# Kernel optimization log

Measured on AMD Instinct MI355X. Metric: run time of the kernel, lower is better.

## Reference

```python
import jax, jax.numpy as jnp
import numpy as np

N_NODES = 100000
N_EDGES = 1600000
BN_EPS = 1e-5
NUM_LAYER = 20


def setup_inputs() -> dict:
    key = jax.random.key(0)
    ks = jax.random.split(key, 10)
    inp = {
        "M": jax.random.normal(ks[0], (N_NODES, 3), dtype=jnp.float32),
        "H": jax.random.normal(ks[1], (N_EDGES, 3), dtype=jnp.float32),
        "edge_index": jax.random.randint(ks[2], (2, N_EDGES), 0, N_NODES, dtype=jnp.int32),
        # mlp_e: Linear(9,4) -> BN(4) -> ReLU -> Linear(4,3)
        "we_w1": jax.random.normal(ks[3], (9, 4), dtype=jnp.float32) * 0.3,
        "we_b1": jnp.zeros((4,), jnp.float32),
        "we_g1": jnp.ones((4,), jnp.float32),
        "we_be1": jnp.zeros((4,), jnp.float32),
        "we_w2": jax.random.normal(ks[4], (4, 3), dtype=jnp.float32) * 0.3,
        "we_b2": jnp.zeros((3,), jnp.float32),
        # mlp_v: Linear(6,3) -> BN(3) -> ReLU -> Linear(3,3)
        "wv_w1": jax.random.normal(ks[5], (6, 3), dtype=jnp.float32) * 0.3,
        "wv_b1": jnp.zeros((3,), jnp.float32),
        "wv_g1": jnp.ones((3,), jnp.float32),
        "wv_be1": jnp.zeros((3,), jnp.float32),
        "wv_w2": jax.random.normal(ks[6], (3, 3), dtype=jnp.float32) * 0.3,
        "wv_b2": jnp.zeros((3,), jnp.float32),
        # head: Linear(3,3) -> BN(3) -> ReLU -> Linear(3,2) -> Softmax
        "out_w1": jax.random.normal(ks[7], (3, 3), dtype=jnp.float32) * 0.3,
        "out_b1": jnp.zeros((3,), jnp.float32),
        "out_g": jnp.ones((3,), jnp.float32),
        "out_be": jnp.zeros((3,), jnp.float32),
        "out_w2": jax.random.normal(ks[8], (3, 2), dtype=jnp.float32) * 0.3,
        "out_b2": jnp.zeros((2,), jnp.float32),
    }
    return inp


def _bn(x, g, b):
    # BatchNorm1d in training mode: batch stats, biased variance
    m = jnp.mean(x, axis=0)
    v = jnp.mean(jnp.square(x - m), axis=0)
    return (x - m) * jax.lax.rsqrt(v + BN_EPS) * g + b


def reference(M, H, edge_index, we_w1, we_b1, we_g1, we_be1, we_w2, we_b2,
              wv_w1, wv_b1, wv_g1, wv_be1, wv_w2, wv_b2,
              out_w1, out_b1, out_g, out_be, out_w2, out_b2):
    src = edge_index[0]  # _j (source, flow=source_to_target)
    dst = edge_index[1]  # _i (target), also the aggregation index
    n = M.shape[0]

    def layer(carry, _):
        M, H = carry
        Mi = M[dst]  # [E,3] gather of target node feats
        Mj = M[src]  # [E,3] gather of source node feats
        e_in = jnp.concatenate([Mi, Mj, H], axis=1)  # [E,9]
        Hn = jax.nn.relu(_bn(e_in @ we_w1 + we_b1, we_g1, we_be1)) @ we_w2 + we_b2  # [E,3]
        v_in = jnp.concatenate([Mi, Hn], axis=1)  # [E,6]
        Mmsg = jax.nn.relu(_bn(v_in @ wv_w1 + wv_b1, wv_g1, wv_be1)) @ wv_w2 + wv_b2  # [E,3]
        Mn = jax.ops.segment_sum(Mmsg, dst, num_segments=n)  # scatter-add to targets
        return (Mn, Hn), None

    (M, H), _ = jax.lax.scan(layer, (M, H), None, length=NUM_LAYER)
    logits = jax.nn.relu(_bn(H @ out_w1 + out_b1, out_g, out_be)) @ out_w2 + out_b2  # [E,2]
    return jax.nn.softmax(logits, axis=1)
```

## Files before the change

kernel.cpp:

```cpp
#include <hip/hip_runtime.h>
#include <hip/hip_fp16.h>
#include <math.h>

#define NNODES 100000
#define NEDGES 1600000
#define NGROUP (NEDGES / 4)
#define NLAYERS 20
#define NB 256
#define BLK 256
#define GRIDE 1024
#define STRIDE (GRIDE * BLK)
#define GRIDL ((NGROUP + BLK - 1) / BLK)
#define NBLKN ((NNODES + 255) / 256)
#define GRIDN4 ((NNODES * 4 + BLK - 1) / BLK)

struct __align__(8) H4 { __half h[4]; };

template<int N>
__device__ __forceinline__ void block_stats_atomic(const float* vals, double* base) {
  __shared__ double sm[16][4];
  int lane = threadIdx.x & 63, wid = threadIdx.x >> 6;
  __syncthreads();
  #pragma unroll
  for (int n = 0; n < N; ++n) {
    double d = (double)vals[n];
    #pragma unroll
    for (int o = 32; o > 0; o >>= 1) d += __shfl_down(d, o, 64);
    if (lane == 0) sm[n][wid] = d;
  }
  __syncthreads();
  if (threadIdx.x < N) {
    double s = sm[threadIdx.x][0] + sm[threadIdx.x][1] + sm[threadIdx.x][2] + sm[threadIdx.x][3];
    atomicAdd(base + threadIdx.x, s);
  }
}

template<int NS>
__device__ __forceinline__ void bank_reduce(const double* __restrict__ acc, double* res) {
  __shared__ double red[BLK * 8];
  int t = threadIdx.x;
  #pragma unroll
  for (int s = 0; s < NS; ++s) red[t * 8 + s] = acc[t * 8 + s];
  __syncthreads();
  for (int o = BLK / 2; o > 0; o >>= 1) {
    if (t < o) {
      #pragma unroll
      for (int s = 0; s < NS; ++s) red[t * 8 + s] += red[(t + o) * 8 + s];
    }
    __syncthreads();
  }
  #pragma unroll
  for (int s = 0; s < NS; ++s) res[s] = red[s];
  __syncthreads();
}

__device__ __forceinline__ void compute_x(const float4 mi, const float4 mj,
    float h0, float h1, float h2,
    const float* __restrict__ w, const float* __restrict__ b, float* x) {
  #pragma unroll
  for (int j = 0; j < 4; ++j) {
    float t = b[j];
    t += mi.x * w[0 * 4 + j]; t += mi.y * w[1 * 4 + j]; t += mi.z * w[2 * 4 + j];
    t += mj.x * w[3 * 4 + j]; t += mj.y * w[4 * 4 + j]; t += mj.z * w[5 * 4 + j];
    t += h0 * w[6 * 4 + j];  t += h1 * w[7 * 4 + j];  t += h2 * w[8 * 4 + j];
    x[j] = t;
  }
}

__global__ void __launch_bounds__(BLK) kz(const float* __restrict__ Min,
                                          float* __restrict__ M,
                                          int* __restrict__ hist,
                                          double* __restrict__ accs) {
  int tid = blockIdx.x * BLK + threadIdx.x;
  for (int v = tid; v < NNODES; v += STRIDE) {
    float4 m;
    m.x = Min[3 * v]; m.y = Min[3 * v + 1]; m.z = Min[3 * v + 2]; m.w = 0.f;
    *(float4*)(M + 4 * (size_t)v) = m;
    hist[v] = 0;
  }
  for (int i = tid; i < 3 * NB * 8; i += STRIDE) accs[i] = 0.0;
}

__global__ void __launch_bounds__(BLK) khr(const int* __restrict__ dst,
                                           int* __restrict__ hist,
                                           int* __restrict__ rankpos) {
  int g = blockIdx.x * BLK + threadIdx.x;
  if (g >= NGROUP) return;
  int4 d4 = ((const int4*)dst)[g];
  int4 r;
  r.x = atomicAdd(&hist[d4.x], 1);
  r.y = atomicAdd(&hist[d4.y], 1);
  r.z = atomicAdd(&hist[d4.z], 1);
  r.w = atomicAdd(&hist[d4.w], 1);
  ((int4*)rankpos)[g] = r;
}

__global__ void __launch_bounds__(256) ksA(const int* __restrict__ hist,
                                           int* __restrict__ bsum) {
  __shared__ int sm[256];
  int i = blockIdx.x * 256 + threadIdx.x;
  sm[threadIdx.x] = (i < NNODES) ? hist[i] : 0;
  __syncthreads();
  for (int o = 128; o > 0; o >>= 1) {
    if (threadIdx.x < o) sm[threadIdx.x] += sm[threadIdx.x + o];
    __syncthreads();
  }
  if (threadIdx.x == 0) bsum[blockIdx.x] = sm[0];
}

__global__ void __launch_bounds__(512) ksB(const int* __restrict__ bsum,
                                           int* __restrict__ bbase) {
  __shared__ int sm[512];
  int t = threadIdx.x;
  sm[t] = (t < NBLKN) ? bsum[t] : 0;
  __syncthreads();
  for (int o = 1; o < 512; o <<= 1) {
    int v = (t >= o) ? sm[t - o] : 0;
    __syncthreads();
    sm[t] += v;
    __syncthreads();
  }
  if (t < NBLKN) bbase[t] = (t == 0) ? 0 : sm[t - 1];
}

__global__ void __launch_bounds__(256) ksC(const int* __restrict__ hist,
                                           const int* __restrict__ bbase,
                                           int* __restrict__ off) {
  __shared__ int sm[256];
  int t = threadIdx.x;
  int i = blockIdx.x * 256 + t;
  int v = (i < NNODES) ? hist[i] : 0;
  sm[t] = v;
  __syncthreads();
  for (int o = 1; o < 256; o <<= 1) {
    int u = (t >= o) ? sm[t - o] : 0;
    __syncthreads();
    sm[t] += u;
    __syncthreads();
  }
  if (i < NNODES) off[i] = bbase[blockIdx.x] + sm[t] - v;
  if (i == 0) off[NNODES] = NEDGES;
}

__global__ void __launch_bounds__(BLK) kd(const int* __restrict__ off,
                                          int* __restrict__ dp) {
  int v = blockIdx.x * BLK + threadIdx.x;
  if (v >= NNODES) return;
  int e0 = off[v], e1 = off[v + 1];
  for (int e = e0; e < e1; ++e) dp[e] = v;
}

__global__ void __launch_bounds__(BLK) kp1(const int* __restrict__ dst,
                                           const int* __restrict__ off,
                                           int* __restrict__ rankpos,
                                           int* __restrict__ eperm) {
  int g = blockIdx.x * BLK + threadIdx.x;
  if (g >= NGROUP) return;
  int4 d4 = ((const int4*)dst)[g];
  int4 r4 = ((int4*)rankpos)[g];
  int4 p4;
  p4.x = off[d4.x] + r4.x;
  p4.y = off[d4.y] + r4.y;
  p4.z = off[d4.z] + r4.z;
  p4.w = off[d4.w] + r4.w;
  int e = 4 * g;
  eperm[p4.x] = e; eperm[p4.y] = e + 1; eperm[p4.z] = e + 2; eperm[p4.w] = e + 3;
  ((int4*)rankpos)[g] = p4;
}

__global__ void __launch_bounds__(BLK) kp2(const int* __restrict__ src,
                                           const float* __restrict__ Hin,
                                           const int* __restrict__ eperm,
                                           int* __restrict__ sp,
                                           __half* __restrict__ Hp) {
  int g = blockIdx.x * BLK + threadIdx.x;
  if (g >= NGROUP) return;
  int4 e4 = ((const int4*)eperm)[g];
  int4 s4;
  s4.x = src[e4.x];
  s4.y = src[e4.y];
  s4.z = src[e4.z];
  s4.w = src[e4.w];
  __half hh[12];
  int ee[4] = {e4.x, e4.y, e4.z, e4.w};
  #pragma unroll
  for (int k = 0; k < 4; ++k) {
    size_t e3 = 3 * (size_t)ee[k];
    hh[3 * k]     = __float2half(Hin[e3]);
    hh[3 * k + 1] = __float2half(Hin[e3 + 1]);
    hh[3 * k + 2] = __float2half(Hin[e3 + 2]);
  }
  ((int4*)sp)[g] = s4;
  H4* Hv = (H4*)(Hp + 12 * (size_t)g);
  H4 a, b, c;
  #pragma unroll
  for (int i = 0; i < 4; ++i) { a.h[i] = hh[i]; b.h[i] = hh[4 + i]; c.h[i] = hh[8 + i]; }
  Hv[0] = a; Hv[1] = b; Hv[2] = c;
}

__global__ void __launch_bounds__(BLK) k1(
    const float* __restrict__ M, const __half* __restrict__ H,
    const int* __restrict__ sp, const int* __restrict__ dp,
    const float* __restrict__ W1, const float* __restrict__ b1,
    double* __restrict__ acc1, double* __restrict__ acc2) {
  int g = blockIdx.x * BLK + threadIdx.x;
  if (blockIdx.x == 0)
    for (int i = threadIdx.x; i < NB * 8; i += BLK) acc2[i] = 0.0;

  float sx[4] = {0, 0, 0, 0}, sq[4] = {0, 0, 0, 0};
  if (g < NGROUP) {
    int4 s4 = ((const int4*)sp)[g];
    int4 d4 = ((const int4*)dp)[g];
    const H4* Hv = (const H4*)(H + 12 * (size_t)g);
    H4 a = Hv[0], b = Hv[1], c = Hv[2];
    float hf[12];
    #pragma unroll
    for (int i = 0; i < 4; ++i) {
      hf[i] = __half2float(a.h[i]); hf[4 + i] = __half2float(b.h[i]); hf[8 + i] = __half2float(c.h[i]);
    }
    float4 mi0 = *(const float4*)(M + 4 * (size_t)d4.x);
    float4 mj0 = *(const float4*)(M + 4 * (size_t)s4.x);
    float4 mi1 = *(const float4*)(M + 4 * (size_t)d4.y);
    float4 mj1 = *(const float4*)(M + 4 * (size_t)s4.y);
    float4 mi2 = *(const float4*)(M + 4 * (size_t)d4.z);
    float4 mj2 = *(const float4*)(M + 4 * (size_t)s4.z);
    float4 mi3 = *(const float4*)(M + 4 * (size_t)d4.w);
    float4 mj3 = *(const float4*)(M + 4 * (size_t)s4.w);
    float x[4][4];
    compute_x(mi0, mj0, hf[0], hf[1], hf[2],  W1, b1, x[0]);
    compute_x(mi1, mj1, hf[3], hf[4], hf[5],  W1, b1, x[1]);
    compute_x(mi2, mj2, hf[6], hf[7], hf[8],  W1, b1, x[2]);
    compute_x(mi3, mj3, hf[9], hf[10], hf[11], W1, b1, x[3]);
    #pragma unroll
    for (int k = 0; k < 4; ++k)
      #pragma unroll
      for (int j = 0; j < 4; ++j) { sx[j] += x[k][j]; sq[j] += x[k][j] * x[k][j]; }
  }
  float vals[8] = {sx[0], sx[1], sx[2], sx[3], sq[0], sq[1], sq[2], sq[3]};
  block_stats_atomic<8>(vals, acc1 + (size_t)(blockIdx.x & (NB - 1)) * 8);
}

__global__ void __launch_bounds__(BLK) k2(
    const float* __restrict__ M, const __half* __restrict__ H, __half* __restrict__ Hn,
    const int* __restrict__ sp, const int* __restrict__ dp,
    const float* __restrict__ W1, const float* __restrict__ b1,
    const float* __restrict__ g1, const float* __restrict__ be1,
    const float* __restrict__ W2, const float* __restrict__ b2,
    const float* __restrict__ V1, const float* __restrict__ vb1,
    const double* __restrict__ acc1, double* __restrict__ acc2,
    int isFinal,
    const float* __restrict__ OW1, const float* __restrict__ ob1,
    double* __restrict__ accF) {
  double red[8];
  bank_reduce<8>(acc1, red);
  float s1[4], t1[4];
  {
    const double invE = 1.0 / (double)NEDGES;
    #pragma unroll
    for (int j = 0; j < 4; ++j) {
      double m = red[j] * invE;
      double var = red[4 + j] * invE - m * m;
      double sc = (double)g1[j] / sqrt(var + 1e-5);
      s1[j] = (float)sc;
      t1[j] = (float)((double)be1[j] - m * sc);
    }
  }
  float sz[3] = {0, 0, 0}, szz[3] = {0, 0, 0}, sf[3] = {0, 0, 0}, sff[3] = {0, 0, 0};
  int g = blockIdx.x * BLK + threadIdx.x;
  if (g < NGROUP) {
    int4 s4 = ((const int4*)sp)[g];
    int4 d4 = ((const int4*)dp)[g];
    const H4* Hv = (const H4*)(H + 12 * (size_t)g);
    H4 ha = Hv[0], hb = Hv[1], hc = Hv[2];
    float hf[12];
    #pragma unroll
    for (int i = 0; i < 4; ++i) {
      hf[i] = __half2float(ha.h[i]); hf[4 + i] = __half2float(hb.h[i]); hf[8 + i] = __half2float(hc.h[i]);
    }
    float4 mi[4], mj[4];
    mi[0] = *(const float4*)(M + 4 * (size_t)d4.x);
    mj[0] = *(const float4*)(M + 4 * (size_t)s4.x);
    mi[1] = *(const float4*)(M + 4 * (size_t)d4.y);
    mj[1] = *(const float4*)(M + 4 * (size_t)s4.y);
    mi[2] = *(const float4*)(M + 4 * (size_t)d4.z);
    mj[2] = *(const float4*)(M + 4 * (size_t)s4.z);
    mi[3] = *(const float4*)(M + 4 * (size_t)d4.w);
    mj[3] = *(const float4*)(M + 4 * (size_t)s4.w);
    __half hh[12];
    float hnr[4][3];
    #pragma unroll
    for (int k = 0; k < 4; ++k) {
      float x[4], y[4];
      compute_x(mi[k], mj[k], hf[3 * k], hf[3 * k + 1], hf[3 * k + 2], W1, b1, x);
      #pragma unroll
      for (int j = 0; j < 4; ++j) y[j] = fmaxf(x[j] * s1[j] + t1[j], 0.f);
      #pragma unroll
      for (int c = 0; c < 3; ++c) {
        float v = b2[c] + y[0] * W2[0 * 3 + c] + y[1] * W2[1 * 3 + c]
                        + y[2] * W2[2 * 3 + c] + y[3] * W2[3 * 3 + c];
        __half hv = __float2half(v);
        hh[3 * k + c] = hv;
        hnr[k][c] = __half2float(hv);
      }
      #pragma unroll
      for (int c = 0; c < 3; ++c) {
        float z = vb1[c] + mi[k].x * V1[0 * 3 + c] + mi[k].y * V1[1 * 3 + c] + mi[k].z * V1[2 * 3 + c]
                         + hnr[k][0] * V1[3 * 3 + c] + hnr[k][1] * V1[4 * 3 + c] + hnr[k][2] * V1[5 * 3 + c];
        sz[c] += z; szz[c] += z * z;
      }
      if (isFinal) {
        #pragma unroll
        for (int c = 0; c < 3; ++c) {
          float f = ob1[c] + hnr[k][0] * OW1[0 * 3 + c] + hnr[k][1] * OW1[1 * 3 + c] + hnr[k][2] * OW1[2 * 3 + c];
          sf[c] += f; sff[c] += f * f;
        }
      }
    }
    H4* Hw = (H4*)(Hn + 12 * (size_t)g);
    H4 oA, oB, oC;
    #pragma unroll
    for (int i = 0; i < 4; ++i) { oA.h[i] = hh[i]; oB.h[i] = hh[4 + i]; oC.h[i] = hh[8 + i]; }
    Hw[0] = oA; Hw[1] = oB; Hw[2] = oC;
  }
  size_t bank = (size_t)(blockIdx.x & (NB - 1)) * 8;
  float v6[6] = {sz[0], sz[1], sz[2], szz[0], szz[1], szz[2]};
  block_stats_atomic<6>(v6, acc2 + bank);
  if (isFinal) {
    float v6b[6] = {sf[0], sf[1], sf[2], sff[0], sff[1], sff[2]};
    block_stats_atomic<6>(v6b, accF + bank);
  }
}

__global__ void __launch_bounds__(BLK) k3(
    const float* __restrict__ M, const __half* __restrict__ Hn,
    const int* __restrict__ off,
    const float* __restrict__ V1, const float* __restrict__ vb1,
    const float* __restrict__ vg1, const float* __restrict__ vbe1,
    const float* __restrict__ V2, const float* __restrict__ vb2,
    const double* __restrict__ acc2, double* __restrict__ acc1,
    float* __restrict__ Mnew) {
  double red[6];
  bank_reduce<6>(acc2, red);
  float s2[3], t2[3];
  {
    const double invE = 1.0 / (double)NEDGES;
    #pragma unroll
    for (int c = 0; c < 3; ++c) {
      double m = red[c] * invE;
      double var = red[3 + c] * invE - m * m;
      double sc = (double)vg1[c] / sqrt(var + 1e-5);
      s2[c] = (float)sc;
      t2[c] = (float)((double)vbe1[c] - m * sc);
    }
  }
  if (blockIdx.x == 0)
    for (int i = threadIdx.x; i < NB * 8; i += BLK) acc1[i] = 0.0;

  int idx = blockIdx.x * BLK + threadIdx.x;
  int v = idx >> 2, q = idx & 3;
  if (v >= NNODES) return;
  float4 mi = *(const float4*)(M + 4 * (size_t)v);
  int e0 = off[v], e1 = off[v + 1];
  float a0 = 0.f, a1 = 0.f, a2v = 0.f;
  for (int e = e0 + q; e < e1; e += 4) {
    size_t e3 = 3 * (size_t)e;
    float h0 = __half2float(Hn[e3]), h1 = __half2float(Hn[e3 + 1]), h2 = __half2float(Hn[e3 + 2]);
    float y[3];
    #pragma unroll
    for (int c = 0; c < 3; ++c) {
      float z = vb1[c] + mi.x * V1[0 * 3 + c] + mi.y * V1[1 * 3 + c] + mi.z * V1[2 * 3 + c]
                       + h0 * V1[3 * 3 + c] + h1 * V1[4 * 3 + c] + h2 * V1[5 * 3 + c];
      y[c] = fmaxf(z * s2[c] + t2[c], 0.f);
    }
    a0  += vb2[0] + y[0] * V2[0] + y[1] * V2[3] + y[2] * V2[6];
    a1  += vb2[1] + y[0] * V2[1] + y[1] * V2[4] + y[2] * V2[7];
    a2v += vb2[2] + y[0] * V2[2] + y[1] * V2[5] + y[2] * V2[8];
  }
  a0  += __shfl_down(a0, 2, 4);  a0  += __shfl_down(a0, 1, 4);
  a1  += __shfl_down(a1, 2, 4);  a1  += __shfl_down(a1, 1, 4);
  a2v += __shfl_down(a2v, 2, 4); a2v += __shfl_down(a2v, 1, 4);
  if (q == 0) {
    float4 o; o.x = a0; o.y = a1; o.z = a2v; o.w = 0.f;
    *(float4*)(Mnew + 4 * (size_t)v) = o;
  }
}

__global__ void __launch_bounds__(BLK) f2(
    const __half* __restrict__ H, const int* __restrict__ pos,
    const float* __restrict__ OW1, const float* __restrict__ ob1,
    const float* __restrict__ og, const float* __restrict__ obe,
    const float* __restrict__ OW2, const float* __restrict__ ob2,
    const double* __restrict__ accF, float* __restrict__ out) {
  double red[6];
  bank_reduce<6>(accF, red);
  float sF[3], tF[3];
  {
    const double invE = 1.0 / (double)NEDGES;
    #pragma unroll
    for (int c = 0; c < 3; ++c) {
      double m = red[c] * invE;
      double var = red[3 + c] * invE - m * m;
      double sc = (double)og[c] / sqrt(var + 1e-5);
      sF[c] = (float)sc;
      tF[c] = (float)((double)obe[c] - m * sc);
    }
  }
  int g = blockIdx.x * BLK + threadIdx.x;
  if (g >= NGROUP) return;
  int4 p4 = ((const int4*)pos)[g];
  int p[4] = {p4.x, p4.y, p4.z, p4.w};
  float2 o[4];
  #pragma unroll
  for (int k = 0; k < 4; ++k) {
    size_t p3 = 3 * (size_t)p[k];
    float h0 = __half2float(H[p3]), h1 = __half2float(H[p3 + 1]), h2 = __half2float(H[p3 + 2]);
    float y[3];
    #pragma unroll
    for (int c = 0; c < 3; ++c) {
      float f = ob1[c] + h0 * OW1[0 * 3 + c] + h1 * OW1[1 * 3 + c] + h2 * OW1[2 * 3 + c];
      y[c] = fmaxf(f * sF[c] + tF[c], 0.f);
    }
    float l0 = ob2[0] + y[0] * OW2[0] + y[1] * OW2[2] + y[2] * OW2[4];
    float l1 = ob2[1] + y[0] * OW2[1] + y[1] * OW2[3] + y[2] * OW2[5];
    float mx = fmaxf(l0, l1);
    float e0 = __expf(l0 - mx), e1 = __expf(l1 - mx);
    float inv = 1.f / (e0 + e1);
    o[k].x = e0 * inv; o[k].y = e1 * inv;
  }
  float4 oA, oB;
  oA.x = o[0].x; oA.y = o[0].y; oA.z = o[1].x; oA.w = o[1].y;
  oB.x = o[2].x; oB.y = o[2].y; oB.z = o[3].x; oB.w = o[3].y;
  ((float4*)out)[2 * (size_t)g] = oA;
  ((float4*)out)[2 * (size_t)g + 1] = oB;
}

extern "C" void kernel_launch(void* const* d_in, const int* in_sizes, int n_in,
                              void* d_out, int out_size, void* d_ws, size_t ws_size,
                              hipStream_t stream) {
  const float* M_in   = (const float*)d_in[0];
  const float* H_in   = (const float*)d_in[1];
  const int*   ei     = (const int*)d_in[2];
  const float* we_w1  = (const float*)d_in[3];
  const float* we_b1  = (const float*)d_in[4];
  const float* we_g1  = (const float*)d_in[5];
  const float* we_be1 = (const float*)d_in[6];
  const float* we_w2  = (const float*)d_in[7];
  const float* we_b2  = (const float*)d_in[8];
  const float* wv_w1  = (const float*)d_in[9];
  const float* wv_b1  = (const float*)d_in[10];
  const float* wv_g1  = (const float*)d_in[11];
  const float* wv_be1 = (const float*)d_in[12];
  const float* wv_w2  = (const float*)d_in[13];
  const float* wv_b2  = (const float*)d_in[14];
  const float* out_w1 = (const float*)d_in[15];
  const float* out_b1 = (const float*)d_in[16];
  const float* out_g  = (const float*)d_in[17];
  const float* out_be = (const float*)d_in[18];
  const float* out_w2 = (const float*)d_in[19];
  const float* out_b2 = (const float*)d_in[20];
  const int* src = ei;
  const int* dst = ei + NEDGES;

  float* ws = (float*)d_ws;
  float* MA  = ws;
  float* MB  = ws + 400000;
  __half* Hp0 = (__half*)(ws + 800000);
  __half* Hp1 = (__half*)(ws + 3200000);
  int* eperm  = (int*)Hp1;
  int* ib      = (int*)(ws + 5600000);
  int* sp      = ib;
  int* dp      = ib + 1600000;
  int* rankpos = ib + 3200000;
  int* hist    = ib + 4800000;
  int* off     = ib + 4900000;
  int* bsum    = ib + 5000001;
  int* bbase   = ib + 5000401;
  double* accs = (double*)(ws + 5600000 + 5000802);
  double* acc1 = accs;
  double* acc2 = accs + NB * 8;
  double* accF = accs + 2 * NB * 8;

  kz<<<GRIDE, BLK, 0, stream>>>(M_in, MA, hist, accs);
  khr<<<GRIDL, BLK, 0, stream>>>(dst, hist, rankpos);
  ksA<<<NBLKN, 256, 0, stream>>>(hist, bsum);
  ksB<<<1, 512, 0, stream>>>(bsum, bbase);
  ksC<<<NBLKN, 256, 0, stream>>>(hist, bbase, off);
  kd<<<NBLKN, BLK, 0, stream>>>(off, dp);
  kp1<<<GRIDL, BLK, 0, stream>>>(dst, off, rankpos, eperm);
  kp2<<<GRIDL, BLK, 0, stream>>>(src, H_in, eperm, sp, Hp0);

  for (int l = 0; l < NLAYERS; ++l) {
    const float* Mc = (l & 1) ? MB : MA;
    float*       Mn = (l & 1) ? MA : MB;
    const __half* Hc = (l & 1) ? Hp1 : Hp0;
    __half*       Hw = (l & 1) ? Hp0 : Hp1;
    k1<<<GRIDL, BLK, 0, stream>>>(Mc, Hc, sp, dp, we_w1, we_b1, acc1, acc2);
    k2<<<GRIDL, BLK, 0, stream>>>(Mc, Hc, Hw, sp, dp, we_w1, we_b1, we_g1, we_be1,
                                  we_w2, we_b2, wv_w1, wv_b1, acc1, acc2,
                                  (l == NLAYERS - 1) ? 1 : 0, out_w1, out_b1, accF);
    if (l < NLAYERS - 1)
      k3<<<GRIDN4, BLK, 0, stream>>>(
          Mc, Hw, off, wv_w1, wv_b1, wv_g1, wv_be1, wv_w2, wv_b2, acc2, acc1, Mn);
  }
  f2<<<GRIDL, BLK, 0, stream>>>(Hp0, rankpos, out_w1, out_b1, out_g, out_be,
                                out_w2, out_b2, accF, (float*)d_out);
}
```

Before: 1.224 ms.

## Delta-pack sorted destination indices and use wave-shuffle bank reduction

Destination indices, which are sorted by CSR order, are packed per group of four as a base plus three 8-bit deltas (int2 instead of int4), halving the dst index traffic read by k1 and k2 on every layer. The dp fill is merged into the scan kernel ksC, removing the separate kd launch, and a new kpk kernel builds the packed array once. bank_reduce replaces the shared-memory tree reduction with wave shuffles plus a 4-entry partial sum, cutting barriers and shared memory. The packing assumes in-group deltas fit in 8 bits, which holds because dp is sorted and a node would need over 255 in-degree gaps to break it; in fact deltas are bounded by node gaps within four consecutive sorted edges, which could exceed 255 only with long runs of empty nodes.

```diff
diff --git a/kernel.cpp b/kernel.cpp
--- a/kernel.cpp
+++ b/kernel.cpp
@@ -37,21 +37,23 @@
 
 template<int NS>
 __device__ __forceinline__ void bank_reduce(const double* __restrict__ acc, double* res) {
-  __shared__ double red[BLK * 8];
+  __shared__ double part[4][8];
   int t = threadIdx.x;
-  #pragma unroll
-  for (int s = 0; s < NS; ++s) red[t * 8 + s] = acc[t * 8 + s];
+  double v[NS];
+  #pragma unroll
+  for (int s = 0; s < NS; ++s) v[s] = acc[t * 8 + s];
+  #pragma unroll
+  for (int o = 32; o > 0; o >>= 1)
+    #pragma unroll
+    for (int s = 0; s < NS; ++s) v[s] += __shfl_down(v[s], o, 64);
+  if ((t & 63) == 0) {
+    int w = t >> 6;
+    #pragma unroll
+    for (int s = 0; s < NS; ++s) part[w][s] = v[s];
+  }
   __syncthreads();
-  for (int o = BLK / 2; o > 0; o >>= 1) {
-    if (t < o) {
-      #pragma unroll
-      for (int s = 0; s < NS; ++s) red[t * 8 + s] += red[(t + o) * 8 + s];
-    }
-    __syncthreads();
-  }
-  #pragma unroll
-  for (int s = 0; s < NS; ++s) res[s] = red[s];
-  __syncthreads();
+  #pragma unroll
+  for (int s = 0; s < NS; ++s) res[s] = part[0][s] + part[1][s] + part[2][s] + part[3][s];
 }
 
 __device__ __forceinline__ void compute_x(const float4 mi, const float4 mj,
@@ -125,7 +127,8 @@
 
 __global__ void __launch_bounds__(256) ksC(const int* __restrict__ hist,
                                            const int* __restrict__ bbase,
-                                           int* __restrict__ off) {
+                                           int* __restrict__ off,
+                                           int* __restrict__ dp) {
   __shared__ int sm[256];
   int t = threadIdx.x;
   int i = blockIdx.x * 256 + t;
@@ -138,16 +141,23 @@
     sm[t] += u;
     __syncthreads();
   }
-  if (i < NNODES) off[i] = bbase[blockIdx.x] + sm[t] - v;
+  if (i < NNODES) {
+    int ex = bbase[blockIdx.x] + sm[t] - v;
+    off[i] = ex;
+    for (int e = ex; e < ex + v; ++e) dp[e] = i;
+  }
   if (i == 0) off[NNODES] = NEDGES;
 }
 
-__global__ void __launch_bounds__(BLK) kd(const int* __restrict__ off,
-                                          int* __restrict__ dp) {
-  int v = blockIdx.x * BLK + threadIdx.x;
-  if (v >= NNODES) return;
-  int e0 = off[v], e1 = off[v + 1];
-  for (int e = e0; e < e1; ++e) dp[e] = v;
+__global__ void __launch_bounds__(BLK) kpk(const int* __restrict__ dp,
+                                           int2* __restrict__ dpp) {
+  int g = blockIdx.x * BLK + threadIdx.x;
+  if (g >= NGROUP) return;
+  int4 d4 = ((const int4*)dp)[g];
+  int2 o;
+  o.x = d4.x;
+  o.y = (d4.y - d4.x) | ((d4.z - d4.x) << 8) | ((d4.w - d4.x) << 16);
+  dpp[g] = o;
 }
 
 __global__ void __launch_bounds__(BLK) kp1(const int* __restrict__ dst,
@@ -200,7 +210,7 @@
 
 __global__ void __launch_bounds__(BLK) k1(
     const float* __restrict__ M, const __half* __restrict__ H,
-    const int* __restrict__ sp, const int* __restrict__ dp,
+    const int* __restrict__ sp, const int2* __restrict__ dpp,
     const float* __restrict__ W1, const float* __restrict__ b1,
     double* __restrict__ acc1, double* __restrict__ acc2) {
   int g = blockIdx.x * BLK + threadIdx.x;
@@ -210,7 +220,11 @@
   float sx[4] = {0, 0, 0, 0}, sq[4] = {0, 0, 0, 0};
   if (g < NGROUP) {
     int4 s4 = ((const int4*)sp)[g];
-    int4 d4 = ((const int4*)dp)[g];
+    int2 dppg = dpp[g];
+    int d0 = dppg.x;
+    int d1 = d0 + (dppg.y & 255);
+    int d2 = d0 + ((dppg.y >> 8) & 255);
+    int d3 = d0 + ((dppg.y >> 16) & 255);
     const H4* Hv = (const H4*)(H + 12 * (size_t)g);
     H4 a = Hv[0], b = Hv[1], c = Hv[2];
     float hf[12];
@@ -218,13 +232,13 @@
     for (int i = 0; i < 4; ++i) {
       hf[i] = __half2float(a.h[i]); hf[4 + i] = __half2float(b.h[i]); hf[8 + i] = __half2float(c.h[i]);
     }
-    float4 mi0 = *(const float4*)(M + 4 * (size_t)d4.x);
+    float4 mi0 = *(const float4*)(M + 4 * (size_t)d0);
     float4 mj0 = *(const float4*)(M + 4 * (size_t)s4.x);
-    float4 mi1 = *(const float4*)(M + 4 * (size_t)d4.y);
+    float4 mi1 = *(const float4*)(M + 4 * (size_t)d1);
     float4 mj1 = *(const float4*)(M + 4 * (size_t)s4.y);
-    float4 mi2 = *(const float4*)(M + 4 * (size_t)d4.z);
+    float4 mi2 = *(const float4*)(M + 4 * (size_t)d2);
     float4 mj2 = *(const float4*)(M + 4 * (size_t)s4.z);
-    float4 mi3 = *(const float4*)(M + 4 * (size_t)d4.w);
+    float4 mi3 = *(const float4*)(M + 4 * (size_t)d3);
     float4 mj3 = *(const float4*)(M + 4 * (size_t)s4.w);
     float x[4][4];
     compute_x(mi0, mj0, hf[0], hf[1], hf[2],  W1, b1, x[0]);
@@ -242,7 +256,7 @@
 
 __global__ void __launch_bounds__(BLK) k2(
     const float* __restrict__ M, const __half* __restrict__ H, __half* __restrict__ Hn,
-    const int* __restrict__ sp, const int* __restrict__ dp,
+    const int* __restrict__ sp, const int2* __restrict__ dpp,
     const float* __restrict__ W1, const float* __restrict__ b1,
     const float* __restrict__ g1, const float* __restrict__ be1,
     const float* __restrict__ W2, const float* __restrict__ b2,
@@ -269,7 +283,12 @@
   int g = blockIdx.x * BLK + threadIdx.x;
   if (g < NGROUP) {
     int4 s4 = ((const int4*)sp)[g];
-    int4 d4 = ((const int4*)dp)[g];
+    int2 dppg = dpp[g];
+    int dd[4];
+    dd[0] = dppg.x;
+    dd[1] = dd[0] + (dppg.y & 255);
+    dd[2] = dd[0] + ((dppg.y >> 8) & 255);
+    dd[3] = dd[0] + ((dppg.y >> 16) & 255);
     const H4* Hv = (const H4*)(H + 12 * (size_t)g);
     H4 ha = Hv[0], hb = Hv[1], hc = Hv[2];
     float hf[12];
@@ -278,13 +297,13 @@
       hf[i] = __half2float(ha.h[i]); hf[4 + i] = __half2float(hb.h[i]); hf[8 + i] = __half2float(hc.h[i]);
     }
     float4 mi[4], mj[4];
-    mi[0] = *(const float4*)(M + 4 * (size_t)d4.x);
+    mi[0] = *(const float4*)(M + 4 * (size_t)dd[0]);
     mj[0] = *(const float4*)(M + 4 * (size_t)s4.x);
-    mi[1] = *(const float4*)(M + 4 * (size_t)d4.y);
+    mi[1] = *(const float4*)(M + 4 * (size_t)dd[1]);
     mj[1] = *(const float4*)(M + 4 * (size_t)s4.y);
-    mi[2] = *(const float4*)(M + 4 * (size_t)d4.z);
+    mi[2] = *(const float4*)(M + 4 * (size_t)dd[2]);
     mj[2] = *(const float4*)(M + 4 * (size_t)s4.z);
-    mi[3] = *(const float4*)(M + 4 * (size_t)d4.w);
+    mi[3] = *(const float4*)(M + 4 * (size_t)dd[3]);
     mj[3] = *(const float4*)(M + 4 * (size_t)s4.w);
     __half hh[12];
     float hnr[4][3];
@@ -471,11 +490,12 @@
   int* sp      = ib;
   int* dp      = ib + 1600000;
   int* rankpos = ib + 3200000;
-  int* hist    = ib + 4800000;
-  int* off     = ib + 4900000;
-  int* bsum    = ib + 5000001;
-  int* bbase   = ib + 5000401;
-  double* accs = (double*)(ws + 5600000 + 5000802);
+  int2* dpp    = (int2*)(ib + 4800000);
+  int* hist    = ib + 5600000;
+  int* off     = ib + 5700000;
+  int* bsum    = ib + 5800001;
+  int* bbase   = ib + 5800401;
+  double* accs = (double*)(ws + 5600000 + 5800802);
   double* acc1 = accs;
   double* acc2 = accs + NB * 8;
   double* accF = accs + 2 * NB * 8;
@@ -484,8 +504,8 @@
   khr<<<GRIDL, BLK, 0, stream>>>(dst, hist, rankpos);
   ksA<<<NBLKN, 256, 0, stream>>>(hist, bsum);
   ksB<<<1, 512, 0, stream>>>(bsum, bbase);
-  ksC<<<NBLKN, 256, 0, stream>>>(hist, bbase, off);
-  kd<<<NBLKN, BLK, 0, stream>>>(off, dp);
+  ksC<<<NBLKN, 256, 0, stream>>>(hist, bbase, off, dp);
+  kpk<<<GRIDL, BLK, 0, stream>>>(dp, dpp);
   kp1<<<GRIDL, BLK, 0, stream>>>(dst, off, rankpos, eperm);
   kp2<<<GRIDL, BLK, 0, stream>>>(src, H_in, eperm, sp, Hp0);
 
@@ -494,8 +514,8 @@
     float*       Mn = (l & 1) ? MA : MB;
     const __half* Hc = (l & 1) ? Hp1 : Hp0;
     __half*       Hw = (l & 1) ? Hp0 : Hp1;
-    k1<<<GRIDL, BLK, 0, stream>>>(Mc, Hc, sp, dp, we_w1, we_b1, acc1, acc2);
-    k2<<<GRIDL, BLK, 0, stream>>>(Mc, Hc, Hw, sp, dp, we_w1, we_b1, we_g1, we_be1,
+    k1<<<GRIDL, BLK, 0, stream>>>(Mc, Hc, sp, dpp, we_w1, we_b1, acc1, acc2);
+    k2<<<GRIDL, BLK, 0, stream>>>(Mc, Hc, Hw, sp, dpp, we_w1, we_b1, we_g1, we_be1,
                                   we_w2, we_b2, wv_w1, wv_b1, acc1, acc2,
                                   (l == NLAYERS - 1) ? 1 : 0, out_w1, out_b1, accF);
     if (l < NLAYERS - 1)
```

Result: faster. 1.170 ms (-4.4%).
